# Kernel optimization log

Hardware: AMD Instinct MI355X
Metric: run time of the kernel (lower is better)

## Reference

```python
import jax, jax.numpy as jnp
import numpy as np

B, T = 4096, 2048
H1, H2 = 32, 16
N_IN, N_OUT = 1, 1


def setup_inputs() -> dict:
    key = jax.random.key(0)
    ks = jax.random.split(key, 12)
    s1 = 1.0 / np.sqrt(H1)  # PyTorch LSTMCell init scale
    s2 = 1.0 / np.sqrt(H2)
    so = 1.0 / np.sqrt(H2)
    return {
        "x": jax.random.normal(ks[0], (B, T, N_IN), dtype=jnp.float32),
        "W_ih1": jax.random.normal(ks[1], (4 * H1, N_IN), dtype=jnp.float32) * s1,
        "W_hh1": jax.random.normal(ks[2], (4 * H1, H1), dtype=jnp.float32) * s1,
        "b_ih1": jax.random.normal(ks[3], (4 * H1,), dtype=jnp.float32) * s1,
        "b_hh1": jax.random.normal(ks[4], (4 * H1,), dtype=jnp.float32) * s1,
        "W_ih2": jax.random.normal(ks[5], (4 * H2, H1), dtype=jnp.float32) * s2,
        "W_hh2": jax.random.normal(ks[6], (4 * H2, H2), dtype=jnp.float32) * s2,
        "b_ih2": jax.random.normal(ks[7], (4 * H2,), dtype=jnp.float32) * s2,
        "b_hh2": jax.random.normal(ks[8], (4 * H2,), dtype=jnp.float32) * s2,
        "W_out": jax.random.normal(ks[9], (N_OUT, H2), dtype=jnp.float32) * so,
        "b_out": jax.random.normal(ks[10], (N_OUT,), dtype=jnp.float32) * so,
    }


def _lstm_cell(x, h, c, W_ih, W_hh, b_ih, b_hh):
    # gates: [B, 4H], PyTorch gate order i, f, g, o
    gates = x @ W_ih.T + b_ih + h @ W_hh.T + b_hh
    i, f, g, o = jnp.split(gates, 4, axis=-1)
    c_new = jax.nn.sigmoid(f) * c + jax.nn.sigmoid(i) * jnp.tanh(g)
    h_new = jax.nn.sigmoid(o) * jnp.tanh(c_new)
    return h_new, c_new


def reference(x, W_ih1, W_hh1, b_ih1, b_hh1, W_ih2, W_hh2, b_ih2, b_hh2, W_out, b_out):
    b = x.shape[0]
    h1 = jnp.zeros((b, H1), x.dtype)
    c1 = jnp.zeros((b, H1), x.dtype)
    h2 = jnp.zeros((b, H2), x.dtype)
    c2 = jnp.zeros((b, H2), x.dtype)

    def step(carry, x_t):
        h1, c1, h2, c2 = carry
        h1, c1 = _lstm_cell(x_t, h1, c1, W_ih1, W_hh1, b_ih1, b_hh1)
        h2, c2 = _lstm_cell(h1, h2, c2, W_ih2, W_hh2, b_ih2, b_hh2)
        y = h2 @ W_out.T + b_out  # [B, n_output]
        return (h1, c1, h2, c2), y

    xs = jnp.swapaxes(x, 0, 1)  # [T, B, n_input]
    _, ys = jax.lax.scan(step, (h1, c1, h2, c2), xs)
    return jnp.swapaxes(ys, 0, 1)  # [B, T, n_output]
```

## Files before the change

### kernel.cpp

```cpp
#include <hip/hip_runtime.h>

#define B_  4096
#define T_  2048
#define H1_ 32
#define H2_ 16
#define RPB 4
#define RPW 2

#define LOG2E     1.44269504088896340736f
#define TWOLOG2E  2.88539008177792681472f

typedef float f32x2 __attribute__((ext_vector_type(2)));
typedef float f32x4 __attribute__((ext_vector_type(4)));

#if defined(__has_builtin)
#if __has_builtin(__builtin_elementwise_fma)
#define PKFMA(acc, a, b) (acc) = __builtin_elementwise_fma((a), (b), (acc))
#endif
#endif
#ifndef PKFMA
#define PKFMA(acc, a, b) (acc) = (a) * (b) + (acc)
#endif

#define FENCE_HW() asm volatile("s_waitcnt lgkmcnt(0)" ::: "memory")
#define FENCE_SW() asm volatile("" ::: "memory")

__device__ __forceinline__ float sig_core(float z) {
    return __builtin_amdgcn_rcpf(1.0f + __builtin_amdgcn_exp2f(-z));
}

#define WS_W1   0
#define WS_W2A  4096
#define WS_W2B  6144
#define WS_WX   7168
#define WS_B1   7296
#define WS_B2   7424
#define WS_N    7488

__device__ __forceinline__ float scale1(int r) {
    return (r >= 64 && r < 96) ? TWOLOG2E : LOG2E;
}
__device__ __forceinline__ float scale2(int r) {
    return ((r >> 4) == 2) ? TWOLOG2E : LOG2E;
}

__global__ __launch_bounds__(256) void prescale_kernel(
    const float* __restrict__ W_ih1, const float* __restrict__ W_hh1,
    const float* __restrict__ b_ih1, const float* __restrict__ b_hh1,
    const float* __restrict__ W_ih2, const float* __restrict__ W_hh2,
    const float* __restrict__ b_ih2, const float* __restrict__ b_hh2,
    float* __restrict__ ws)
{
    const int i = blockIdx.x * 256 + threadIdx.x;
    if (i >= WS_N) return;
    float v;
    if (i < WS_W2A) {
        v = W_hh1[i] * scale1(i >> 5);
    } else if (i < WS_W2B) {
        const int j = i - WS_W2A;
        v = W_ih2[j] * scale2(j >> 5);
    } else if (i < WS_WX) {
        const int j = i - WS_W2B;
        v = W_hh2[j] * scale2(j >> 4);
    } else if (i < WS_B1) {
        const int r = i - WS_WX;
        v = W_ih1[r] * scale1(r);
    } else if (i < WS_B2) {
        const int r = i - WS_B1;
        v = (b_ih1[r] + b_hh1[r]) * scale1(r);
    } else {
        const int r = i - WS_B2;
        v = (b_ih2[r] + b_hh2[r]) * scale2(r);
    }
    ws[i] = v;
}

__global__ __launch_bounds__(64 * RPB, 2) void lstm_deep_kernel(
    const float* __restrict__ x,
    const float* __restrict__ ws,
    const float* __restrict__ W_out,
    const float* __restrict__ b_out,
    float* __restrict__ out)
{
    const int tid  = threadIdx.x;
    const int lane = tid & 63;
    const int wid  = tid >> 6;
    const int row0 = (blockIdx.x * RPB + wid) * RPW;
    const int row1 = row0 + 1;

    __shared__ __align__(16) float sh1[RPB][RPW][H1_];
    __shared__ __align__(16) float sh2[RPB][RPW][2][H2_];

    const int ga = lane;
    const int gb = 64 + lane;

    const f32x2* W1p  = reinterpret_cast<const f32x2*>(ws + WS_W1);
    const f32x2* W2ap = reinterpret_cast<const f32x2*>(ws + WS_W2A);
    const f32x2* W2bp = reinterpret_cast<const f32x2*>(ws + WS_W2B);

    f32x2 w1a[H1_ / 2], w1b[H1_ / 2];
    #pragma unroll
    for (int j = 0; j < H1_ / 2; ++j) {
        w1a[j] = W1p[ga * (H1_ / 2) + j];
        w1b[j] = W1p[gb * (H1_ / 2) + j];
    }
    f32x2 w2a[H1_ / 2];
    #pragma unroll
    for (int j = 0; j < H1_ / 2; ++j) w2a[j] = W2ap[lane * (H1_ / 2) + j];
    f32x2 w2b[H2_ / 2];
    #pragma unroll
    for (int j = 0; j < H2_ / 2; ++j) w2b[j] = W2bp[lane * (H2_ / 2) + j];

    float wxa = ws[WS_WX + ga];
    float wxb = ws[WS_WX + gb];
    float ba  = ws[WS_B1 + ga];
    float bb  = ws[WS_B1 + gb];
    float b2  = ws[WS_B2 + lane];

    #pragma unroll
    for (int j = 0; j < H1_ / 2; ++j)
        asm volatile("" : "+v"(w1a[j]), "+v"(w1b[j]), "+v"(w2a[j]));
    #pragma unroll
    for (int j = 0; j < H2_ / 2; ++j)
        asm volatile("" : "+v"(w2b[j]));
    asm volatile("" : "+v"(wxa), "+v"(wxb), "+v"(ba), "+v"(bb), "+v"(b2));

    const bool  low  = (lane < 32);
    const int   gt   = lane >> 4;
    const float sc1b = low ? 2.0f : 1.0f;
    const float of1b = low ? -1.0f : 0.0f;
    const float sc2c = (gt == 2) ? 2.0f : 1.0f;
    const float of2c = (gt == 2) ? -1.0f : 0.0f;

    const int   u2   = lane & 15;
    const float wout = W_out[u2];
    const float bout = b_out[0];

    float c1_0 = 0.0f, c1_1 = 0.0f;
    float c2_0 = 0.0f, c2_1 = 0.0f;
    if (lane < H1_) { sh1[wid][0][lane] = 0.0f; sh1[wid][1][lane] = 0.0f; }
    if (lane < H2_) {
        sh2[wid][0][0][lane] = 0.0f; sh2[wid][0][1][lane] = 0.0f;
        sh2[wid][1][0][lane] = 0.0f; sh2[wid][1][1][lane] = 0.0f;
    }
    FENCE_HW();

    const f32x4* __restrict__ xr0  = reinterpret_cast<const f32x4*>(x + (size_t)row0 * T_);
    const f32x4* __restrict__ xr1  = reinterpret_cast<const f32x4*>(x + (size_t)row1 * T_);
    float*       __restrict__ or0  = out + (size_t)row0 * T_;
    float*       __restrict__ or1  = out + (size_t)row1 * T_;

    auto step2 = [&](float xt0, float xt1, int par, float& yp0, float& yp1) {
        f32x2 A0 = {__builtin_fmaf(wxa, xt0, ba), 0.0f};
        f32x2 B0 = {__builtin_fmaf(wxb, xt0, bb), 0.0f};
        f32x2 A1 = {__builtin_fmaf(wxa, xt1, ba), 0.0f};
        f32x2 B1 = {__builtin_fmaf(wxb, xt1, bb), 0.0f};
        {
            const f32x4* p0 = reinterpret_cast<const f32x4*>(sh1[wid][0]);
            const f32x4* p1 = reinterpret_cast<const f32x4*>(sh1[wid][1]);
            #pragma unroll
            for (int q = 0; q < H1_ / 4; ++q) {
                const f32x4 v0 = p0[q];
                const f32x4 v1 = p1[q];
                const f32x2 a01 = {v0.x, v0.y}, a23 = {v0.z, v0.w};
                const f32x2 b01 = {v1.x, v1.y}, b23 = {v1.z, v1.w};
                PKFMA(A0, w1a[2 * q],     a01);
                PKFMA(A1, w1a[2 * q],     b01);
                PKFMA(B0, w1b[2 * q],     a01);
                PKFMA(B1, w1b[2 * q],     b01);
                PKFMA(A0, w1a[2 * q + 1], a23);
                PKFMA(A1, w1a[2 * q + 1], b23);
                PKFMA(B0, w1b[2 * q + 1], a23);
                PKFMA(B1, w1b[2 * q + 1], b23);
            }
        }

        f32x2 E0 = {b2, 0.0f}, F0 = {0.0f, 0.0f};
        f32x2 E1 = {b2, 0.0f}, F1 = {0.0f, 0.0f};
        {
            const f32x4* q0 = reinterpret_cast<const f32x4*>(sh2[wid][0][par ^ 1]);
            const f32x4* q1 = reinterpret_cast<const f32x4*>(sh2[wid][1][par ^ 1]);
            #pragma unroll
            for (int q = 0; q < H2_ / 4; ++q) {
                const f32x4 v0 = q0[q];
                const f32x4 v1 = q1[q];
                const f32x2 va01 = {v0.x, v0.y}, va23 = {v0.z, v0.w};
                const f32x2 vb01 = {v1.x, v1.y}, vb23 = {v1.z, v1.w};
                PKFMA(E0, w2b[2 * q],     va01);
                PKFMA(E1, w2b[2 * q],     vb01);
                PKFMA(F0, w2b[2 * q + 1], va23);
                PKFMA(F1, w2b[2 * q + 1], vb23);
            }
        }

        const float acca0 = A0.x + A0.y, accb0 = B0.x + B0.y;
        const float acca1 = A1.x + A1.y, accb1 = B1.x + B1.y;

        const float sa0 = sig_core(acca0);
        const float sa1 = sig_core(acca1);
        const float sb0 = __builtin_fmaf(sc1b, sig_core(accb0), of1b);
        const float sb1 = __builtin_fmaf(sc1b, sig_core(accb1), of1b);
        const float pv0 = __shfl_xor(sa0 * sb0, 32);
        const float pv1 = __shfl_xor(sa1 * sb1, 32);
        c1_0 = __builtin_fmaf(sa0, c1_0, pv0);
        c1_1 = __builtin_fmaf(sa1, c1_1, pv1);
        const float tc10 = __builtin_fmaf(2.0f, sig_core(TWOLOG2E * c1_0), -1.0f);
        const float tc11 = __builtin_fmaf(2.0f, sig_core(TWOLOG2E * c1_1), -1.0f);
        const float h1n0 = sb0 * tc10;
        const float h1n1 = sb1 * tc11;

        if (lane >= 32) {
            sh1[wid][0][lane - 32] = h1n0;
            sh1[wid][1][lane - 32] = h1n1;
        }
        FENCE_HW();

        {
            const f32x4* p0 = reinterpret_cast<const f32x4*>(sh1[wid][0]);
            const f32x4* p1 = reinterpret_cast<const f32x4*>(sh1[wid][1]);
            #pragma unroll
            for (int q = 0; q < H1_ / 4; ++q) {
                const f32x4 v0 = p0[q];
                const f32x4 v1 = p1[q];
                const f32x2 va01 = {v0.x, v0.y}, va23 = {v0.z, v0.w};
                const f32x2 vb01 = {v1.x, v1.y}, vb23 = {v1.z, v1.w};
                PKFMA(E0, w2a[2 * q],     va01);
                PKFMA(E1, w2a[2 * q],     vb01);
                PKFMA(F0, w2a[2 * q + 1], va23);
                PKFMA(F1, w2a[2 * q + 1], vb23);
            }
        }
        const float d20 = (E0.x + E0.y) + (F0.x + F0.y);
        const float d21 = (E1.x + E1.y) + (F1.x + F1.y);

        const float s20 = __builtin_fmaf(sc2c, sig_core(d20), of2c);
        const float s21 = __builtin_fmaf(sc2c, sig_core(d21), of2c);
        const float t320 = s20 * __shfl_xor(s20, 32);
        const float t321 = s21 * __shfl_xor(s21, 32);
        const float sf0  = __shfl(s20, u2 + 16), sf1 = __shfl(s21, u2 + 16);
        const float so0  = __shfl(s20, u2 + 48), so1 = __shfl(s21, u2 + 48);

        c2_0 = __builtin_fmaf(sf0, c2_0, t320);
        c2_1 = __builtin_fmaf(sf1, c2_1, t321);
        const float tc20 = __builtin_fmaf(2.0f, sig_core(TWOLOG2E * c2_0), -1.0f);
        const float tc21 = __builtin_fmaf(2.0f, sig_core(TWOLOG2E * c2_1), -1.0f);
        const float h2v0 = so0 * tc20;
        const float h2v1 = so1 * tc21;

        if (lane < H2_) {
            sh2[wid][0][par][lane] = h2v0;
            sh2[wid][1][par][lane] = h2v1;
        }
        FENCE_SW();

        yp0 = wout * h2v0;
        yp1 = wout * h2v1;
    };

    f32x4 xv0 = xr0[0];
    f32x4 xv1 = xr1[0];
    #pragma unroll 1
    for (int t4 = 0; t4 < T_ / 4; ++t4) {
        const int nx = (t4 + 1 < T_ / 4) ? (t4 + 1) : t4;
        const f32x4 xn0 = xr0[nx];
        const f32x4 xn1 = xr1[nx];

        float p00, p10, p01, p11, p02, p12, p03, p13;
        step2(xv0.x, xv1.x, 0, p00, p10);
        step2(xv0.y, xv1.y, 1, p01, p11);
        step2(xv0.z, xv1.z, 0, p02, p12);
        step2(xv0.w, xv1.w, 1, p03, p13);

        #pragma unroll
        for (int off = 1; off <= 8; off <<= 1) {
            p00 += __shfl_xor(p00, off);  p10 += __shfl_xor(p10, off);
            p01 += __shfl_xor(p01, off);  p11 += __shfl_xor(p11, off);
            p02 += __shfl_xor(p02, off);  p12 += __shfl_xor(p12, off);
            p03 += __shfl_xor(p03, off);  p13 += __shfl_xor(p13, off);
        }

        if (lane == 0) {
            f32x4 y0 = {p00 + bout, p01 + bout, p02 + bout, p03 + bout};
            f32x4 y1 = {p10 + bout, p11 + bout, p12 + bout, p13 + bout};
            *reinterpret_cast<f32x4*>(or0 + 4 * t4) = y0;
            *reinterpret_cast<f32x4*>(or1 + 4 * t4) = y1;
        }
        xv0 = xn0;
        xv1 = xn1;
    }
}

extern "C" void kernel_launch(void* const* d_in, const int* in_sizes, int n_in,
                              void* d_out, int out_size, void* d_ws, size_t ws_size,
                              hipStream_t stream) {
    const float* xp     = (const float*)d_in[0];
    const float* W_ih1  = (const float*)d_in[1];
    const float* W_hh1  = (const float*)d_in[2];
    const float* b_ih1  = (const float*)d_in[3];
    const float* b_hh1  = (const float*)d_in[4];
    const float* W_ih2  = (const float*)d_in[5];
    const float* W_hh2  = (const float*)d_in[6];
    const float* b_ih2  = (const float*)d_in[7];
    const float* b_hh2  = (const float*)d_in[8];
    const float* W_out  = (const float*)d_in[9];
    const float* b_out  = (const float*)d_in[10];
    float* out = (float*)d_out;
    float* ws  = (float*)d_ws;

    prescale_kernel<<<(WS_N + 255) / 256, 256, 0, stream>>>(
        W_ih1, W_hh1, b_ih1, b_hh1, W_ih2, W_hh2, b_ih2, b_hh2, ws);

    dim3 grid(B_ / (RPB * RPW));
    dim3 block(64 * RPB);
    lstm_deep_kernel<<<grid, block, 0, stream>>>(xp, ws, W_out, b_out, out);
}
```

Baseline: 2.422 ms.

## Software-pipeline layer-1 matvec into layer-2 pass and keep h2 in registers

Each step now reads the shared h1 vector once and computes both the layer-2 input matvec and the next step's layer-1 recurrent matvec from it, so the next step's layer-1 gates are precomputed. Layer-2 hidden state moves out of LDS into per-lane register arrays, filled by broadcasting with readlane, which removes the double-buffered sh2 and its reads. Some index shuffles become xor shuffles. The cost is 32 readlane instructions per step and more register pressure, plus removal of the explicit sh1 zero-init, which relies on the first step's h1 write before it is read.

Result: faster. 2.257 ms (-6.8%).

```diff
diff --git a/kernel.cpp b/kernel.cpp
--- a/kernel.cpp
+++ b/kernel.cpp
@@ -27,6 +27,9 @@
 
 __device__ __forceinline__ float sig_core(float z) {
     return __builtin_amdgcn_rcpf(1.0f + __builtin_amdgcn_exp2f(-z));
+}
+__device__ __forceinline__ float lane_bcast(float v, int srcLane) {
+    return __uint_as_float(__builtin_amdgcn_readlane(__float_as_uint(v), srcLane));
 }
 
 #define WS_W1   0
@@ -89,7 +92,6 @@
     const int row1 = row0 + 1;
 
     __shared__ __align__(16) float sh1[RPB][RPW][H1_];
-    __shared__ __align__(16) float sh2[RPB][RPW][2][H2_];
 
     const int ga = lane;
     const int gb = 64 + lane;
@@ -138,63 +140,25 @@
 
     float c1_0 = 0.0f, c1_1 = 0.0f;
     float c2_0 = 0.0f, c2_1 = 0.0f;
-    if (lane < H1_) { sh1[wid][0][lane] = 0.0f; sh1[wid][1][lane] = 0.0f; }
-    if (lane < H2_) {
-        sh2[wid][0][0][lane] = 0.0f; sh2[wid][0][1][lane] = 0.0f;
-        sh2[wid][1][0][lane] = 0.0f; sh2[wid][1][1][lane] = 0.0f;
-    }
-    FENCE_HW();
-
-    const f32x4* __restrict__ xr0  = reinterpret_cast<const f32x4*>(x + (size_t)row0 * T_);
-    const f32x4* __restrict__ xr1  = reinterpret_cast<const f32x4*>(x + (size_t)row1 * T_);
-    float*       __restrict__ or0  = out + (size_t)row0 * T_;
-    float*       __restrict__ or1  = out + (size_t)row1 * T_;
-
-    auto step2 = [&](float xt0, float xt1, int par, float& yp0, float& yp1) {
-        f32x2 A0 = {__builtin_fmaf(wxa, xt0, ba), 0.0f};
-        f32x2 B0 = {__builtin_fmaf(wxb, xt0, bb), 0.0f};
-        f32x2 A1 = {__builtin_fmaf(wxa, xt1, ba), 0.0f};
-        f32x2 B1 = {__builtin_fmaf(wxb, xt1, bb), 0.0f};
-        {
-            const f32x4* p0 = reinterpret_cast<const f32x4*>(sh1[wid][0]);
-            const f32x4* p1 = reinterpret_cast<const f32x4*>(sh1[wid][1]);
-            #pragma unroll
-            for (int q = 0; q < H1_ / 4; ++q) {
-                const f32x4 v0 = p0[q];
-                const f32x4 v1 = p1[q];
-                const f32x2 a01 = {v0.x, v0.y}, a23 = {v0.z, v0.w};
-                const f32x2 b01 = {v1.x, v1.y}, b23 = {v1.z, v1.w};
-                PKFMA(A0, w1a[2 * q],     a01);
-                PKFMA(A1, w1a[2 * q],     b01);
-                PKFMA(B0, w1b[2 * q],     a01);
-                PKFMA(B1, w1b[2 * q],     b01);
-                PKFMA(A0, w1a[2 * q + 1], a23);
-                PKFMA(A1, w1a[2 * q + 1], b23);
-                PKFMA(B0, w1b[2 * q + 1], a23);
-                PKFMA(B1, w1b[2 * q + 1], b23);
-            }
-        }
-
-        f32x2 E0 = {b2, 0.0f}, F0 = {0.0f, 0.0f};
-        f32x2 E1 = {b2, 0.0f}, F1 = {0.0f, 0.0f};
-        {
-            const f32x4* q0 = reinterpret_cast<const f32x4*>(sh2[wid][0][par ^ 1]);
-            const f32x4* q1 = reinterpret_cast<const f32x4*>(sh2[wid][1][par ^ 1]);
-            #pragma unroll
-            for (int q = 0; q < H2_ / 4; ++q) {
-                const f32x4 v0 = q0[q];
-                const f32x4 v1 = q1[q];
-                const f32x2 va01 = {v0.x, v0.y}, va23 = {v0.z, v0.w};
-                const f32x2 vb01 = {v1.x, v1.y}, vb23 = {v1.z, v1.w};
-                PKFMA(E0, w2b[2 * q],     va01);
-                PKFMA(E1, w2b[2 * q],     vb01);
-                PKFMA(F0, w2b[2 * q + 1], va23);
-                PKFMA(F1, w2b[2 * q + 1], vb23);
-            }
-        }
-
-        const float acca0 = A0.x + A0.y, accb0 = B0.x + B0.y;
-        const float acca1 = A1.x + A1.y, accb1 = B1.x + B1.y;
+    float h2s0[H2_], h2s1[H2_];
+    #pragma unroll
+    for (int k = 0; k < H2_; ++k) { h2s0[k] = 0.0f; h2s1[k] = 0.0f; }
+
+    const f32x4* __restrict__ xr0 = reinterpret_cast<const f32x4*>(x + (size_t)row0 * T_);
+    const f32x4* __restrict__ xr1 = reinterpret_cast<const f32x4*>(x + (size_t)row1 * T_);
+    float*       __restrict__ or0 = out + (size_t)row0 * T_;
+    float*       __restrict__ or1 = out + (size_t)row1 * T_;
+
+    f32x4 xv0 = xr0[0];
+    f32x4 xv1 = xr1[0];
+    f32x2 A0c = {__builtin_fmaf(wxa, xv0.x, ba), 0.0f};
+    f32x2 B0c = {__builtin_fmaf(wxb, xv0.x, bb), 0.0f};
+    f32x2 A1c = {__builtin_fmaf(wxa, xv1.x, ba), 0.0f};
+    f32x2 B1c = {__builtin_fmaf(wxb, xv1.x, bb), 0.0f};
+
+    auto step2 = [&](float nxt0, float nxt1, float& yp0, float& yp1) {
+        const float acca0 = A0c.x + A0c.y, accb0 = B0c.x + B0c.y;
+        const float acca1 = A1c.x + A1c.y, accb1 = B1c.x + B1c.y;
 
         const float sa0 = sig_core(acca0);
         const float sa1 = sig_core(acca1);
@@ -213,7 +177,27 @@
             sh1[wid][0][lane - 32] = h1n0;
             sh1[wid][1][lane - 32] = h1n1;
         }
+
+        f32x2 E0 = {b2, 0.0f}, F0 = {0.0f, 0.0f};
+        f32x2 E1 = {b2, 0.0f}, F1 = {0.0f, 0.0f};
+        #pragma unroll
+        for (int q = 0; q < H2_ / 4; ++q) {
+            const f32x2 hA0 = {h2s0[4 * q],     h2s0[4 * q + 1]};
+            const f32x2 hB0 = {h2s0[4 * q + 2], h2s0[4 * q + 3]};
+            const f32x2 hA1 = {h2s1[4 * q],     h2s1[4 * q + 1]};
+            const f32x2 hB1 = {h2s1[4 * q + 2], h2s1[4 * q + 3]};
+            PKFMA(E0, w2b[2 * q],     hA0);
+            PKFMA(F0, w2b[2 * q + 1], hB0);
+            PKFMA(E1, w2b[2 * q],     hA1);
+            PKFMA(F1, w2b[2 * q + 1], hB1);
+        }
+
         FENCE_HW();
+
+        A0c = f32x2{__builtin_fmaf(wxa, nxt0, ba), 0.0f};
+        B0c = f32x2{__builtin_fmaf(wxb, nxt0, bb), 0.0f};
+        A1c = f32x2{__builtin_fmaf(wxa, nxt1, ba), 0.0f};
+        B1c = f32x2{__builtin_fmaf(wxb, nxt1, bb), 0.0f};
 
         {
             const f32x4* p0 = reinterpret_cast<const f32x4*>(sh1[wid][0]);
@@ -222,12 +206,20 @@
             for (int q = 0; q < H1_ / 4; ++q) {
                 const f32x4 v0 = p0[q];
                 const f32x4 v1 = p1[q];
-                const f32x2 va01 = {v0.x, v0.y}, va23 = {v0.z, v0.w};
-                const f32x2 vb01 = {v1.x, v1.y}, vb23 = {v1.z, v1.w};
-                PKFMA(E0, w2a[2 * q],     va01);
-                PKFMA(E1, w2a[2 * q],     vb01);
-                PKFMA(F0, w2a[2 * q + 1], va23);
-                PKFMA(F1, w2a[2 * q + 1], vb23);
+                const f32x2 a01 = {v0.x, v0.y}, a23 = {v0.z, v0.w};
+                const f32x2 b01 = {v1.x, v1.y}, b23 = {v1.z, v1.w};
+                PKFMA(E0,  w2a[2 * q],     a01);
+                PKFMA(F0,  w2a[2 * q + 1], a23);
+                PKFMA(E1,  w2a[2 * q],     b01);
+                PKFMA(F1,  w2a[2 * q + 1], b23);
+                PKFMA(A0c, w1a[2 * q],     a01);
+                PKFMA(A0c, w1a[2 * q + 1], a23);
+                PKFMA(B0c, w1b[2 * q],     a01);
+                PKFMA(B0c, w1b[2 * q + 1], a23);
+                PKFMA(A1c, w1a[2 * q],     b01);
+                PKFMA(A1c, w1a[2 * q + 1], b23);
+                PKFMA(B1c, w1b[2 * q],     b01);
+                PKFMA(B1c, w1b[2 * q + 1], b23);
             }
         }
         const float d20 = (E0.x + E0.y) + (F0.x + F0.y);
@@ -237,8 +229,8 @@
         const float s21 = __builtin_fmaf(sc2c, sig_core(d21), of2c);
         const float t320 = s20 * __shfl_xor(s20, 32);
         const float t321 = s21 * __shfl_xor(s21, 32);
-        const float sf0  = __shfl(s20, u2 + 16), sf1 = __shfl(s21, u2 + 16);
-        const float so0  = __shfl(s20, u2 + 48), so1 = __shfl(s21, u2 + 48);
+        const float sf0  = __shfl_xor(s20, 16), sf1 = __shfl_xor(s21, 16);
+        const float so0  = __shfl_xor(s20, 48), so1 = __shfl_xor(s21, 48);
 
         c2_0 = __builtin_fmaf(sf0, c2_0, t320);
         c2_1 = __builtin_fmaf(sf1, c2_1, t321);
@@ -247,9 +239,10 @@
         const float h2v0 = so0 * tc20;
         const float h2v1 = so1 * tc21;
 
-        if (lane < H2_) {
-            sh2[wid][0][par][lane] = h2v0;
-            sh2[wid][1][par][lane] = h2v1;
+        #pragma unroll
+        for (int k = 0; k < H2_; ++k) {
+            h2s0[k] = lane_bcast(h2v0, k);
+            h2s1[k] = lane_bcast(h2v1, k);
         }
         FENCE_SW();
 
@@ -257,8 +250,6 @@
         yp1 = wout * h2v1;
     };
 
-    f32x4 xv0 = xr0[0];
-    f32x4 xv1 = xr1[0];
     #pragma unroll 1
     for (int t4 = 0; t4 < T_ / 4; ++t4) {
         const int nx = (t4 + 1 < T_ / 4) ? (t4 + 1) : t4;
@@ -266,10 +257,10 @@
         const f32x4 xn1 = xr1[nx];
 
         float p00, p10, p01, p11, p02, p12, p03, p13;
-        step2(xv0.x, xv1.x, 0, p00, p10);
-        step2(xv0.y, xv1.y, 1, p01, p11);
-        step2(xv0.z, xv1.z, 0, p02, p12);
-        step2(xv0.w, xv1.w, 1, p03, p13);
+        step2(xv0.y, xv1.y, p00, p10);
+        step2(xv0.z, xv1.z, p01, p11);
+        step2(xv0.w, xv1.w, p02, p12);
+        step2(xn0.x, xn1.x, p03, p13);
 
         #pragma unroll
         for (int off = 1; off <= 8; off <<= 1) {
```
